# Kernel optimization log

Hardware: AMD Instinct MI355X
Metric: run time of the kernel (lower is better)

## Reference

```python
import jax, jax.numpy as jnp
from jax import lax
import numpy as np

N, H, E, K = 8192, 1024, 8, 2


def setup_inputs() -> dict:
    key = jax.random.key(0)
    ks = jax.random.split(key, 6)
    s = 0.02
    return {
        "tokens": jax.random.normal(ks[0], (N, H), dtype=jnp.float32),
        "router_w": jax.random.normal(ks[1], (E, H), dtype=jnp.float32) * s,   # Linear(H,E,bias=False) weight [out,in]
        "w1": jax.random.normal(ks[2], (E, 2 * H, H), dtype=jnp.float32) * s,  # stacked expert fc1 [out,in]
        "b1": jax.random.normal(ks[3], (E, 2 * H), dtype=jnp.float32) * s,
        "w2": jax.random.normal(ks[4], (E, H, 2 * H), dtype=jnp.float32) * s,  # stacked expert fc2
        "b2": jax.random.normal(ks[5], (E, H), dtype=jnp.float32) * s,
    }


def reference(tokens, router_w, w1, b1, w2, b2):
    # Router logits and top-k dispatch weights
    logits = tokens @ router_w.T                      # [N, E]
    scores, idx = lax.top_k(logits, K)                # [N, K]
    probs = jax.nn.softmax(scores, axis=-1)           # softmax over the top-k scores only
    # combine[n, e] = prob if expert e selected for token n else 0
    combine = jnp.zeros((N, E), dtype=tokens.dtype)
    combine = combine.at[jnp.arange(N)[:, None], idx].add(probs)
    # Per-expert MLP (loop over fixed small E; zero combine weight masks non-selected)
    out = jnp.zeros_like(tokens)
    for e in range(E):
        h = jax.nn.gelu(tokens @ w1[e].T + b1[e], approximate=False)  # [N, 2H]
        y = h @ w2[e].T + b2[e]                                       # [N, H]
        out = out + combine[:, e:e + 1] * y
    return out
```

## Files before the change

### kernel.cpp

```cpp
#include <hip/hip_runtime.h>
#include <stdint.h>

#define N_TOK 8192
#define HDIM  1024
#define NEXP  8
#define CAP   16384
#define MAXTILE 136

typedef __bf16 bf16x8 __attribute__((ext_vector_type(8)));
typedef float  f32x4  __attribute__((ext_vector_type(4)));

__device__ inline unsigned short f2bf(float f) {
  union { float f; unsigned u; } v; v.f = f;
  return (unsigned short)((v.u + 0x7fffu + ((v.u >> 16) & 1u)) >> 16);
}

__device__ inline float bf2f(unsigned short b) {
  union { unsigned u; float f; } v; v.u = (unsigned)b << 16; return v.f;
}

__device__ inline float gelu_f(float x) {
  float y = 0.7978845608028654f * (x + 0.044715f * x * x * x);
  y = fminf(fmaxf(y, -15.f), 15.f);
  float t = __expf(2.f * y);
  return 0.5f * x * (1.f + (t - 1.f) / (t + 1.f));
}

__device__ inline void gld_lds16(const void* gptr, void* lptr) {
  __builtin_amdgcn_global_load_lds(
      (const __attribute__((address_space(1))) void*)(uintptr_t)gptr,
      (__attribute__((address_space(3))) void*)(uintptr_t)lptr,
      16, 0, 0);
}

__global__ __launch_bounds__(256) void cvt_kernel(const float* __restrict__ src,
                                                  unsigned short* __restrict__ dst,
                                                  int n4) {
  int i = blockIdx.x * 256 + threadIdx.x;
  int stride = gridDim.x * 256;
  for (; i < n4; i += stride) {
    float4 v = reinterpret_cast<const float4*>(src)[i];
    ushort4 o;
    o.x = f2bf(v.x); o.y = f2bf(v.y); o.z = f2bf(v.z); o.w = f2bf(v.w);
    reinterpret_cast<ushort4*>(dst)[i] = o;
  }
}

__global__ __launch_bounds__(256) void router_kernel(
    const float* __restrict__ tokens, const float* __restrict__ rw,
    unsigned short* __restrict__ tokb, int* __restrict__ pair,
    float* __restrict__ probs) {
  int wid = threadIdx.x >> 6, lane = threadIdx.x & 63;
  int n = blockIdx.x * 4 + wid;
  const float4* trow = (const float4*)(tokens + (size_t)n * HDIM);
  ushort4* tdst = (ushort4*)(tokb + (size_t)n * HDIM);
  float acc[NEXP];
#pragma unroll
  for (int e = 0; e < NEXP; e++) acc[e] = 0.f;
#pragma unroll
  for (int it = 0; it < 4; it++) {
    int c4 = it * 64 + lane;
    float4 tv = trow[c4];
    ushort4 o;
    o.x = f2bf(tv.x); o.y = f2bf(tv.y); o.z = f2bf(tv.z); o.w = f2bf(tv.w);
    tdst[c4] = o;
#pragma unroll
    for (int e = 0; e < NEXP; e++) {
      float4 w = ((const float4*)(rw + e * HDIM))[c4];
      acc[e] += tv.x * w.x + tv.y * w.y + tv.z * w.z + tv.w * w.w;
    }
  }
#pragma unroll
  for (int e = 0; e < NEXP; e++) {
#pragma unroll
    for (int off = 32; off > 0; off >>= 1) acc[e] += __shfl_xor(acc[e], off, 64);
  }
  if (lane == 0) {
    int e0 = 0; float s0 = acc[0];
#pragma unroll
    for (int e = 1; e < NEXP; e++) if (acc[e] > s0) { s0 = acc[e]; e0 = e; }
    int e1 = -1; float s1 = -3.4e38f;
#pragma unroll
    for (int e = 0; e < NEXP; e++) if (e != e0 && acc[e] > s1) { s1 = acc[e]; e1 = e; }
    float z  = expf(s1 - s0);
    float p0 = 1.f / (1.f + z);
    pair[n] = e0 | (e1 << 8);
    probs[2 * n]     = p0;
    probs[2 * n + 1] = z * p0;
  }
}

__global__ __launch_bounds__(1024) void dispatch_kernel(
    const int* __restrict__ pair, int* __restrict__ counts,
    int* __restrict__ rowids) {
  int e = blockIdx.x;
  int t = threadIdx.x;
  __shared__ int sc[1024];
  int p8[8];
  int c = 0;
#pragma unroll
  for (int i = 0; i < 8; i++) {
    p8[i] = pair[t * 8 + i];
    c += ((p8[i] & 255) == e) + (((p8[i] >> 8) & 255) == e);
  }
  sc[t] = c;
  __syncthreads();
  for (int off = 1; off < 1024; off <<= 1) {
    int v = (t >= off) ? sc[t - off] : 0;
    __syncthreads();
    sc[t] += v;
    __syncthreads();
  }
  if (t == 1023) counts[e] = sc[1023];
  int* dst = rowids + e * CAP + (sc[t] - c);
#pragma unroll
  for (int i = 0; i < 8; i++) {
    int n = t * 8 + i;
    if ((p8[i] & 255) == e)        *dst++ = 2 * n;
    if (((p8[i] >> 8) & 255) == e) *dst++ = 2 * n + 1;
  }
}

__global__ void worklist_kernel(const int* __restrict__ counts, int* __restrict__ wl) {
  if (threadIdx.x == 0) {
    int p = 0;
    for (int e = 0; e < NEXP; e++) {
      int nt = (counts[e] + 127) >> 7;
      for (int i = 0; i < nt; i++) { wl[1 + p] = (e << 16) | i; p++; }
    }
    wl[0] = p;
  }
}

template <int MODE>
__global__ __launch_bounds__(256) void moe_gemm(
    const unsigned short* __restrict__ Abase,
    const unsigned short* __restrict__ Wb,
    const float* __restrict__ bias,
    const int* __restrict__ counts, const int* __restrict__ rowids,
    const int* __restrict__ wl, const float* __restrict__ probs,
    unsigned short* __restrict__ dstbuf) {
  constexpr int KT   = MODE ? 16 : 8;
  constexpr int NCOL = MODE ? 1024 : 2048;
  constexpr int KDIM = MODE ? 2048 : 1024;

  int s = blockIdx.x & 7;
  int r = blockIdx.x >> 3;
  int tile, cb;
  if constexpr (MODE == 0) {
    tile = r >> 1;
    cb   = ((r & 1) << 3) + s;
  } else {
    tile = r;
    cb   = s;
  }
  if (tile >= wl[0]) return;
  int d  = wl[1 + tile];
  int e  = d >> 16;
  int rb = d & 0xffff;
  int ce = counts[e];
  const int* rl = rowids + e * CAP + rb * 128;

  int t = threadIdx.x;
  __shared__ __align__(16) char smem[65536];

  int jsrc = (t & 15) ^ ((t >> 4) & 15);
  const char* asrc[8];
  const char* bsrc[8];
#pragma unroll
  for (int i = 0; i < 8; i++) {
    int rr = i * 16 + (t >> 4);
    int rid = (rb * 128 + rr < ce) ? rl[rr] : rl[0];
    long arow = MODE ? (long)rid : (long)(rid >> 1);
    asrc[i] = (const char*)(Abase + arow * KDIM) + jsrc * 16;
    bsrc[i] = (const char*)(Wb + ((long)e * NCOL + cb * 128 + rr) * KDIM) + jsrc * 16;
  }

  f32x4 acc[4][4];
#pragma unroll
  for (int mi = 0; mi < 4; mi++)
#pragma unroll
    for (int ni = 0; ni < 4; ni++) {
      f32x4 z = {0.f, 0.f, 0.f, 0.f};
      acc[mi][ni] = z;
    }

  int lane = t & 63, wid = t >> 6;
  int wr = wid >> 1, wc = wid & 1;
  int lr = lane >> 4, lc = lane & 15;

  for (int kt = 0; kt < KT; kt++) {
#pragma unroll
    for (int i = 0; i < 8; i++)
      gld_lds16(asrc[i] + kt * 256, smem + i * 4096 + t * 16);
#pragma unroll
    for (int i = 0; i < 8; i++)
      gld_lds16(bsrc[i] + kt * 256, smem + 32768 + i * 4096 + t * 16);
    __syncthreads();
#pragma unroll
    for (int ks = 0; ks < 4; ks++) {
      bf16x8 af[4], bfr[4];
      int j = ks * 4 + lr;
#pragma unroll
      for (int mi = 0; mi < 4; mi++) {
        int rr = wr * 64 + mi * 16 + lc;
        af[mi] = *(const bf16x8*)(smem + rr * 256 + ((j ^ (rr & 15)) * 16));
      }
#pragma unroll
      for (int ni = 0; ni < 4; ni++) {
        int rr = wc * 64 + ni * 16 + lc;
        bfr[ni] = *(const bf16x8*)(smem + 32768 + rr * 256 + ((j ^ (rr & 15)) * 16));
      }
      __builtin_amdgcn_s_setprio(1);
#pragma unroll
      for (int mi = 0; mi < 4; mi++)
#pragma unroll
        for (int ni = 0; ni < 4; ni++)
          acc[mi][ni] = __builtin_amdgcn_mfma_f32_16x16x32_bf16(af[mi], bfr[ni], acc[mi][ni], 0, 0, 0);
      __builtin_amdgcn_s_setprio(0);
    }
    __syncthreads();
  }

  float bcol[4];
#pragma unroll
  for (int ni = 0; ni < 4; ni++)
    bcol[ni] = bias[e * NCOL + cb * 128 + wc * 64 + ni * 16 + lc];

#pragma unroll
  for (int mi = 0; mi < 4; mi++) {
#pragma unroll
    for (int r4 = 0; r4 < 4; r4++) {
      int lrow = wr * 64 + mi * 16 + lr * 4 + r4;
      float p = 1.f;
      if constexpr (MODE == 1)
        p = (rb * 128 + lrow < ce) ? probs[rl[lrow]] : 0.f;
#pragma unroll
      for (int ni = 0; ni < 4; ni++) {
        int col = wc * 64 + ni * 16 + lc;
        float x = acc[mi][ni][r4] + bcol[ni];
        if constexpr (MODE == 0)
          x = gelu_f(x);
        else
          x *= p;
        int j = col >> 3;
        *(unsigned short*)(smem + lrow * 256 + ((j ^ (lrow & 15)) << 4) + (col & 7) * 2) = f2bf(x);
      }
    }
  }
  __syncthreads();

  int row = t >> 1, h = t & 1;
  if (rb * 128 + row < ce) {
    int rid = rl[row];
    char* dst = (char*)(dstbuf + (long)rid * NCOL + cb * 128) + h * 128;
#pragma unroll
    for (int i = 0; i < 8; i++) {
      int j = h * 8 + i;
      *(int4*)(dst + i * 16) = *(const int4*)(smem + row * 256 + ((j ^ (row & 15)) << 4));
    }
  }
}

typedef short short8v __attribute__((ext_vector_type(8)));
__global__ __launch_bounds__(256) void merge_kernel(const unsigned short* __restrict__ Y,
                                                    float* __restrict__ out) {
  int i = blockIdx.x * 256 + threadIdx.x;
  int n = i >> 7, c = (i & 127) * 8;
  const short8v a = *(const short8v*)(Y + (long)(2 * n) * HDIM + c);
  const short8v b = *(const short8v*)(Y + (long)(2 * n + 1) * HDIM + c);
  float4 o0, o1;
#pragma unroll
  for (int k = 0; k < 8; k++) {
    float v = bf2f((unsigned short)a[k]) + bf2f((unsigned short)b[k]);
    if (k < 4) (&o0.x)[k] = v; else (&o1.x)[k - 4] = v;
  }
  float4* dst = (float4*)(out + (long)n * HDIM + c);
  dst[0] = o0; dst[1] = o1;
}

extern "C" void kernel_launch(void* const* d_in, const int* in_sizes, int n_in,
                              void* d_out, int out_size, void* d_ws, size_t ws_size,
                              hipStream_t stream) {
  const float* tokens   = (const float*)d_in[0];
  const float* router_w = (const float*)d_in[1];
  const float* w1       = (const float*)d_in[2];
  const float* b1       = (const float*)d_in[3];
  const float* w2       = (const float*)d_in[4];
  const float* b2       = (const float*)d_in[5];
  float* out = (float*)d_out;

  char* ws = (char*)d_ws;
  int*            counts = (int*)ws;
  int*            rowids = (int*)(ws + 64);
  float*          probs  = (float*)(ws + 64 + NEXP * CAP * 4);
  int*            pair   = (int*)(ws + 64 + NEXP * CAP * 4 + N_TOK * 2 * 4);
  int*            wl     = (int*)(ws + 64 + NEXP * CAP * 4 + N_TOK * 2 * 4 + N_TOK * 4);
  unsigned short* tokb   = (unsigned short*)(ws + (1u << 20));
  unsigned short* w1b    = (unsigned short*)(ws + (1u << 20) + 16777216u);
  unsigned short* w2b    = (unsigned short*)(ws + (1u << 20) + 16777216u + 33554432u);
  unsigned short* Hbuf   = (unsigned short*)(ws + (1u << 20) + 16777216u + 67108864u);
  unsigned short* Ybuf   = w1b;

  cvt_kernel<<<2048, 256, 0, stream>>>(w1, w1b, NEXP * 2048 * 1024 / 4);
  cvt_kernel<<<2048, 256, 0, stream>>>(w2, w2b, NEXP * 1024 * 2048 / 4);
  router_kernel<<<N_TOK / 4, 256, 0, stream>>>(tokens, router_w, tokb, pair, probs);
  dispatch_kernel<<<NEXP, 1024, 0, stream>>>(pair, counts, rowids);
  worklist_kernel<<<1, 64, 0, stream>>>(counts, wl);
  moe_gemm<0><<<MAXTILE * 16, 256, 0, stream>>>(tokb, w1b, b1, counts, rowids, wl, probs, Hbuf);
  moe_gemm<1><<<MAXTILE * 8, 256, 0, stream>>>(Hbuf, w2b, b2, counts, rowids, wl, probs, Ybuf);
  merge_kernel<<<N_TOK * HDIM / 8 / 256, 256, 0, stream>>>(Ybuf, out);
}
```

Before: 320.4 us.

## Split fc1 GEMM into dedicated 512-thread kernel with 128x256 tiles

The templated GEMM is split into two kernels. The fc1 kernel now uses 512 threads (8 waves) computing a 128x256 output tile with a K-step of 64 instead of 128. Token rows loaded into LDS are reused across twice as many output columns, and each block is larger. The epilogue writes its two 128-column halves in sequence through LDS with extra barriers, and the smaller K step doubles the number of sync iterations.

```diff
diff --git a/kernel.cpp b/kernel.cpp
--- a/kernel.cpp
+++ b/kernel.cpp
@@ -132,28 +132,17 @@
   }
 }
 
-template <int MODE>
-__global__ __launch_bounds__(256) void moe_gemm(
-    const unsigned short* __restrict__ Abase,
-    const unsigned short* __restrict__ Wb,
-    const float* __restrict__ bias,
+__global__ __launch_bounds__(512) void moe_gemm0(
+    const unsigned short* __restrict__ tokb,
+    const unsigned short* __restrict__ w1b,
+    const float* __restrict__ b1,
     const int* __restrict__ counts, const int* __restrict__ rowids,
-    const int* __restrict__ wl, const float* __restrict__ probs,
-    unsigned short* __restrict__ dstbuf) {
-  constexpr int KT   = MODE ? 16 : 8;
-  constexpr int NCOL = MODE ? 1024 : 2048;
-  constexpr int KDIM = MODE ? 2048 : 1024;
-
-  int s = blockIdx.x & 7;
-  int r = blockIdx.x >> 3;
-  int tile, cb;
-  if constexpr (MODE == 0) {
-    tile = r >> 1;
-    cb   = ((r & 1) << 3) + s;
-  } else {
-    tile = r;
-    cb   = s;
-  }
+    const int* __restrict__ wl,
+    unsigned short* __restrict__ Hbuf) {
+  constexpr int KT = 16;
+
+  int cb   = blockIdx.x & 7;
+  int tile = blockIdx.x >> 3;
   if (tile >= wl[0]) return;
   int d  = wl[1 + tile];
   int e  = d >> 16;
@@ -162,6 +151,126 @@
   const int* rl = rowids + e * CAP + rb * 128;
 
   int t = threadIdx.x;
+  __shared__ __align__(16) char smem[49152];
+
+  int jsrc = (t & 7) ^ ((t >> 3) & 7);
+  const char* asrc[2];
+  const char* bsrc[4];
+#pragma unroll
+  for (int i = 0; i < 2; i++) {
+    int rr = i * 64 + (t >> 3);
+    int rid = (rb * 128 + rr < ce) ? rl[rr] : rl[0];
+    asrc[i] = (const char*)(tokb + (long)(rid >> 1) * HDIM) + jsrc * 16;
+  }
+#pragma unroll
+  for (int i = 0; i < 4; i++) {
+    int rr = i * 64 + (t >> 3);
+    bsrc[i] = (const char*)(w1b + ((long)e * 2048 + cb * 256 + rr) * HDIM) + jsrc * 16;
+  }
+
+  f32x4 acc[4][4];
+#pragma unroll
+  for (int mi = 0; mi < 4; mi++)
+#pragma unroll
+    for (int ni = 0; ni < 4; ni++) {
+      f32x4 z = {0.f, 0.f, 0.f, 0.f};
+      acc[mi][ni] = z;
+    }
+
+  int lane = t & 63, wid = t >> 6;
+  int wr = wid >> 2, wc = wid & 3;
+  int lr = lane >> 4, lc = lane & 15;
+
+  for (int kt = 0; kt < KT; kt++) {
+#pragma unroll
+    for (int i = 0; i < 2; i++)
+      gld_lds16(asrc[i] + kt * 128, smem + i * 8192 + t * 16);
+#pragma unroll
+    for (int i = 0; i < 4; i++)
+      gld_lds16(bsrc[i] + kt * 128, smem + 16384 + i * 8192 + t * 16);
+    __syncthreads();
+#pragma unroll
+    for (int ks = 0; ks < 2; ks++) {
+      bf16x8 af[4], bfv[4];
+      int j = ks * 4 + lr;
+#pragma unroll
+      for (int mi = 0; mi < 4; mi++) {
+        int rr = wr * 64 + mi * 16 + lc;
+        af[mi] = *(const bf16x8*)(smem + rr * 128 + ((j ^ (rr & 7)) << 4));
+      }
+#pragma unroll
+      for (int ni = 0; ni < 4; ni++) {
+        int rr = wc * 64 + ni * 16 + lc;
+        bfv[ni] = *(const bf16x8*)(smem + 16384 + rr * 128 + ((j ^ (rr & 7)) << 4));
+      }
+      __builtin_amdgcn_s_setprio(1);
+#pragma unroll
+      for (int mi = 0; mi < 4; mi++)
+#pragma unroll
+        for (int ni = 0; ni < 4; ni++)
+          acc[mi][ni] = __builtin_amdgcn_mfma_f32_16x16x32_bf16(af[mi], bfv[ni], acc[mi][ni], 0, 0, 0);
+      __builtin_amdgcn_s_setprio(0);
+    }
+    __syncthreads();
+  }
+
+  float bcol[4];
+#pragma unroll
+  for (int ni = 0; ni < 4; ni++)
+    bcol[ni] = b1[e * 2048 + cb * 256 + wc * 64 + ni * 16 + lc];
+
+#pragma unroll
+  for (int h = 0; h < 2; h++) {
+    if ((wc >> 1) == h) {
+#pragma unroll
+      for (int mi = 0; mi < 4; mi++) {
+#pragma unroll
+        for (int r4 = 0; r4 < 4; r4++) {
+          int lrow = wr * 64 + mi * 16 + lr * 4 + r4;
+#pragma unroll
+          for (int ni = 0; ni < 4; ni++) {
+            int colh = (wc & 1) * 64 + ni * 16 + lc;
+            float x = gelu_f(acc[mi][ni][r4] + bcol[ni]);
+            int j = colh >> 3;
+            *(unsigned short*)(smem + lrow * 256 + ((j ^ (lrow & 15)) << 4) + (colh & 7) * 2) = f2bf(x);
+          }
+        }
+      }
+    }
+    __syncthreads();
+    int row = t >> 2, q = t & 3;
+    if (rb * 128 + row < ce) {
+      int rid = rl[row];
+      char* dst = (char*)(Hbuf + (long)rid * 2048 + cb * 256 + h * 128) + q * 64;
+#pragma unroll
+      for (int i = 0; i < 4; i++) {
+        int jj = q * 4 + i;
+        *(int4*)(dst + i * 16) = *(const int4*)(smem + row * 256 + ((jj ^ (row & 15)) << 4));
+      }
+    }
+    __syncthreads();
+  }
+}
+
+__global__ __launch_bounds__(256) void moe_gemm1(
+    const unsigned short* __restrict__ Hbuf,
+    const unsigned short* __restrict__ w2b,
+    const float* __restrict__ b2,
+    const int* __restrict__ counts, const int* __restrict__ rowids,
+    const int* __restrict__ wl, const float* __restrict__ probs,
+    unsigned short* __restrict__ Ybuf) {
+  constexpr int KT = 16;
+
+  int cb   = blockIdx.x & 7;
+  int tile = blockIdx.x >> 3;
+  if (tile >= wl[0]) return;
+  int d  = wl[1 + tile];
+  int e  = d >> 16;
+  int rb = d & 0xffff;
+  int ce = counts[e];
+  const int* rl = rowids + e * CAP + rb * 128;
+
+  int t = threadIdx.x;
   __shared__ __align__(16) char smem[65536];
 
   int jsrc = (t & 15) ^ ((t >> 4) & 15);
@@ -171,9 +280,8 @@
   for (int i = 0; i < 8; i++) {
     int rr = i * 16 + (t >> 4);
     int rid = (rb * 128 + rr < ce) ? rl[rr] : rl[0];
-    long arow = MODE ? (long)rid : (long)(rid >> 1);
-    asrc[i] = (const char*)(Abase + arow * KDIM) + jsrc * 16;
-    bsrc[i] = (const char*)(Wb + ((long)e * NCOL + cb * 128 + rr) * KDIM) + jsrc * 16;
+    asrc[i] = (const char*)(Hbuf + (long)rid * 2048) + jsrc * 16;
+    bsrc[i] = (const char*)(w2b + ((long)e * 1024 + cb * 128 + rr) * 2048) + jsrc * 16;
   }
 
   f32x4 acc[4][4];
@@ -204,12 +312,12 @@
 #pragma unroll
       for (int mi = 0; mi < 4; mi++) {
         int rr = wr * 64 + mi * 16 + lc;
-        af[mi] = *(const bf16x8*)(smem + rr * 256 + ((j ^ (rr & 15)) * 16));
+        af[mi] = *(const bf16x8*)(smem + rr * 256 + ((j ^ (rr & 15)) << 4));
       }
 #pragma unroll
       for (int ni = 0; ni < 4; ni++) {
         int rr = wc * 64 + ni * 16 + lc;
-        bfr[ni] = *(const bf16x8*)(smem + 32768 + rr * 256 + ((j ^ (rr & 15)) * 16));
+        bfr[ni] = *(const bf16x8*)(smem + 32768 + rr * 256 + ((j ^ (rr & 15)) << 4));
       }
       __builtin_amdgcn_s_setprio(1);
 #pragma unroll
@@ -225,24 +333,18 @@
   float bcol[4];
 #pragma unroll
   for (int ni = 0; ni < 4; ni++)
-    bcol[ni] = bias[e * NCOL + cb * 128 + wc * 64 + ni * 16 + lc];
+    bcol[ni] = b2[e * 1024 + cb * 128 + wc * 64 + ni * 16 + lc];
 
 #pragma unroll
   for (int mi = 0; mi < 4; mi++) {
 #pragma unroll
     for (int r4 = 0; r4 < 4; r4++) {
       int lrow = wr * 64 + mi * 16 + lr * 4 + r4;
-      float p = 1.f;
-      if constexpr (MODE == 1)
-        p = (rb * 128 + lrow < ce) ? probs[rl[lrow]] : 0.f;
+      float p = (rb * 128 + lrow < ce) ? probs[rl[lrow]] : 0.f;
 #pragma unroll
       for (int ni = 0; ni < 4; ni++) {
         int col = wc * 64 + ni * 16 + lc;
-        float x = acc[mi][ni][r4] + bcol[ni];
-        if constexpr (MODE == 0)
-          x = gelu_f(x);
-        else
-          x *= p;
+        float x = (acc[mi][ni][r4] + bcol[ni]) * p;
         int j = col >> 3;
         *(unsigned short*)(smem + lrow * 256 + ((j ^ (lrow & 15)) << 4) + (col & 7) * 2) = f2bf(x);
       }
@@ -253,7 +355,7 @@
   int row = t >> 1, h = t & 1;
   if (rb * 128 + row < ce) {
     int rid = rl[row];
-    char* dst = (char*)(dstbuf + (long)rid * NCOL + cb * 128) + h * 128;
+    char* dst = (char*)(Ybuf + (long)rid * 1024 + cb * 128) + h * 128;
 #pragma unroll
     for (int i = 0; i < 8; i++) {
       int j = h * 8 + i;
@@ -307,7 +409,7 @@
   router_kernel<<<N_TOK / 4, 256, 0, stream>>>(tokens, router_w, tokb, pair, probs);
   dispatch_kernel<<<NEXP, 1024, 0, stream>>>(pair, counts, rowids);
   worklist_kernel<<<1, 64, 0, stream>>>(counts, wl);
-  moe_gemm<0><<<MAXTILE * 16, 256, 0, stream>>>(tokb, w1b, b1, counts, rowids, wl, probs, Hbuf);
-  moe_gemm<1><<<MAXTILE * 8, 256, 0, stream>>>(Hbuf, w2b, b2, counts, rowids, wl, probs, Ybuf);
+  moe_gemm0<<<MAXTILE * 8, 512, 0, stream>>>(tokb, w1b, b1, counts, rowids, wl, Hbuf);
+  moe_gemm1<<<MAXTILE * 8, 256, 0, stream>>>(Hbuf, w2b, b2, counts, rowids, wl, probs, Ybuf);
   merge_kernel<<<N_TOK * HDIM / 8 / 256, 256, 0, stream>>>(Ybuf, out);
 }
```

After: 337.1 us. 5.2% more time.
